# Optimization experiments

Measured on AMD Instinct MI355X. Metric: run time of the kernel, lower is better.

Reference implementation:

```python
import jax, jax.numpy as jnp
import numpy as np

EPS = 1e-5
N, K, CIN, COUT = 100000, 27, 64, 128


def sparse_conv(x, nbr, W):
    # x: [N, C]; nbr: [N, K] with sentinel index N meaning 'no neighbor'
    x_pad = jnp.concatenate([x, jnp.zeros((1, x.shape[1]), x.dtype)], axis=0)  # [N+1, C]
    g = x_pad[nbr]  # gather: [N, K, C]
    return jnp.einsum('nkc,kcd->nd', g, W)  # per-offset GEMM, scatter to output sites


def bn_relu(y, gamma, beta):
    # BatchNorm over active sites (training-mode batch statistics), then ReLU
    mu = y.mean(axis=0)
    var = y.var(axis=0)
    return jax.nn.relu((y - mu) * jax.lax.rsqrt(var + EPS) * gamma + beta)


def setup_inputs() -> dict:
    key = jax.random.key(0)
    ks = jax.random.split(key, 5)
    x = jax.random.normal(ks[0], (N, CIN), dtype=jnp.float32)
    # sentinel N indicates missing neighbor (maps to zero-padded row)
    nbr = jax.random.randint(ks[1], (N, K), 0, N + 1)
    W1 = jax.random.normal(ks[2], (K, CIN, COUT), dtype=jnp.float32) * (1.0 / np.sqrt(K * CIN))
    W2 = jax.random.normal(ks[3], (K, COUT, COUT), dtype=jnp.float32) * (1.0 / np.sqrt(K * COUT))
    W_skip = jax.random.normal(ks[4], (CIN, COUT), dtype=jnp.float32) * (1.0 / np.sqrt(CIN))
    return {
        'x': x, 'nbr': nbr,
        'W1': W1, 'gamma1': jnp.ones((COUT,), jnp.float32), 'beta1': jnp.zeros((COUT,), jnp.float32),
        'W2': W2, 'gamma2': jnp.ones((COUT,), jnp.float32), 'beta2': jnp.zeros((COUT,), jnp.float32),
        'W_skip': W_skip,
    }


def reference(x, nbr, W1, gamma1, beta1, W2, gamma2, beta2, W_skip):
    identity = x @ W_skip                      # 1x1 conv skip (same coords)
    h = bn_relu(sparse_conv(x, nbr, W1), gamma1, beta1)
    h = bn_relu(sparse_conv(h, nbr, W2), gamma2, beta2)
    return h + identity
```

## Files before the change

### kernel.cpp

```cpp
#include <hip/hip_runtime.h>
#include <hip/hip_bf16.h>

#define NSITES 100000
#define KOFFS 27
#define CIN 64
#define COUT 128

typedef unsigned short u16;
typedef __attribute__((ext_vector_type(8))) short s16x8;
typedef __attribute__((ext_vector_type(4))) float f32x4;

static __device__ __forceinline__ u16 f2bf(float f) {
    union { float f; unsigned u; } x; x.f = f;
    return (u16)((x.u + 0x7FFFu + ((x.u >> 16) & 1u)) >> 16);
}
static __device__ __forceinline__ float bf2f(u16 v) {
    union { unsigned u; float f; } x; x.u = ((unsigned)v) << 16;
    return x.f;
}

__global__ void prep_kernel(const float* __restrict__ W1, const float* __restrict__ W2,
                            const float* __restrict__ Wsk,
                            u16* __restrict__ W1t, u16* __restrict__ W2t,
                            u16* __restrict__ Wskt, float* __restrict__ zero_area) {
    int i = blockIdx.x * 256 + threadIdx.x;
    if (i < 27 * 64 * 128) {
        int k = i / 8192, r = i & 8191, d = r >> 6, c = r & 63;
        W1t[i] = f2bf(W1[k * 8192 + c * 128 + d]);
        return;
    }
    i -= 27 * 64 * 128;
    if (i < 27 * 128 * 128) {
        int k = i / 16384, r = i & 16383, d = r >> 7, c = r & 127;
        W2t[i] = f2bf(W2[k * 16384 + c * 128 + d]);
        return;
    }
    i -= 27 * 128 * 128;
    if (i < 8192) {
        int d = i >> 6, c = i & 63;
        Wskt[i] = f2bf(Wsk[c * 128 + d]);
        return;
    }
    i -= 8192;
    zero_area[i] = 0.0f;
}

__global__ void convert_x_kernel(const float* __restrict__ x, u16* __restrict__ xb) {
    long long e = ((long long)blockIdx.x * 256 + threadIdx.x) * 8;
    if (e >= (long long)(NSITES + 1) * CIN) return;
    s16x8 o;
    if (e < (long long)NSITES * CIN) {
        float4 v0 = *(const float4*)(x + e);
        float4 v1 = *(const float4*)(x + e + 4);
        o[0] = (short)f2bf(v0.x); o[1] = (short)f2bf(v0.y);
        o[2] = (short)f2bf(v0.z); o[3] = (short)f2bf(v0.w);
        o[4] = (short)f2bf(v1.x); o[5] = (short)f2bf(v1.y);
        o[6] = (short)f2bf(v1.z); o[7] = (short)f2bf(v1.w);
    } else {
#pragma unroll
        for (int j = 0; j < 8; ++j) o[j] = 0;
    }
    *(s16x8*)(xb + e) = o;
}

template <int CK, bool IDENT_FUSE, bool STATS>
__global__ __launch_bounds__(256, 3) void conv_kernel(
    const u16* __restrict__ xin, const int* __restrict__ nbr,
    const u16* __restrict__ Wt, u16* __restrict__ yout,
    float* __restrict__ psum, float* __restrict__ psq, int nk,
    const u16* __restrict__ Wskt, float* __restrict__ outid) {
    constexpr int STRIDE = CK + 8;
    constexpr int KSTEPS = CK / 32;
    constexpr int CPR = CK / 8;
    constexpr int RPP = 256 / CPR;
    constexpr int NPASS = 64 / RPP;
    __shared__ __align__(16) u16 a_tile[64 * STRIDE];
    __shared__ int nbr_tile[64 * KOFFS];

    const int tid = threadIdx.x;
    const int wave = tid >> 6;
    const int lane = tid & 63;
    const int m = lane & 15;
    const int q = lane >> 4;
    const int n0 = blockIdx.x * 64;
    const int wc = wave * 32;
    const int srow = tid / CPR;
    const int schunk = tid % CPR;

    for (int i = tid; i < 64 * KOFFS; i += 256) {
        int r = i / KOFFS;
        int kk = i - r * KOFFS;
        int row = n0 + r;
        nbr_tile[i] = (row < NSITES) ? nbr[row * KOFFS + kk] : NSITES;
    }
    __syncthreads();

    f32x4 acc[4][2];
#pragma unroll
    for (int rt = 0; rt < 4; ++rt)
#pragma unroll
        for (int ct = 0; ct < 2; ++ct)
#pragma unroll
            for (int r = 0; r < 4; ++r) acc[rt][ct][r] = 0.0f;

    s16x8 ag0[NPASS], ag1[NPASS];
#pragma unroll
    for (int p = 0; p < NPASS; ++p) {
        int r = p * RPP + srow;
        ag0[p] = *(const s16x8*)(xin + (long long)nbr_tile[r * KOFFS] * CK + schunk * 8);
    }
    if (nk > 1) {
#pragma unroll
        for (int p = 0; p < NPASS; ++p) {
            int r = p * RPP + srow;
            ag1[p] = *(const s16x8*)(xin + (long long)nbr_tile[r * KOFFS + 1] * CK + schunk * 8);
        }
    }

    auto conv_iter = [&](int k, s16x8 (&agc)[NPASS]) {
        s16x8 bf[2][KSTEPS];
        const u16* wb = Wt + (long long)k * (COUT * CK);
#pragma unroll
        for (int ct = 0; ct < 2; ++ct)
#pragma unroll
            for (int ks = 0; ks < KSTEPS; ++ks)
                bf[ct][ks] = *(const s16x8*)(wb + (wc + ct * 16 + m) * CK + ks * 32 + q * 8);

#pragma unroll
        for (int p = 0; p < NPASS; ++p)
            *(s16x8*)(a_tile + (p * RPP + srow) * STRIDE + schunk * 8) = agc[p];

        if (k + 2 < nk) {
#pragma unroll
            for (int p = 0; p < NPASS; ++p) {
                int r = p * RPP + srow;
                agc[p] = *(const s16x8*)(xin + (long long)nbr_tile[r * KOFFS + k + 2] * CK + schunk * 8);
            }
        }
        __syncthreads();

#pragma unroll
        for (int ks = 0; ks < KSTEPS; ++ks) {
            s16x8 af[4];
#pragma unroll
            for (int rt = 0; rt < 4; ++rt)
                af[rt] = *(const s16x8*)(a_tile + (rt * 16 + m) * STRIDE + ks * 32 + q * 8);
#pragma unroll
            for (int rt = 0; rt < 4; ++rt)
#pragma unroll
                for (int ct = 0; ct < 2; ++ct)
                    acc[rt][ct] = __builtin_amdgcn_mfma_f32_16x16x32_bf16(
                        af[rt], bf[ct][ks], acc[rt][ct], 0, 0, 0);
        }
        __syncthreads();
    };

    for (int k = 0; k < nk; k += 2) {
        conv_iter(k, ag0);
        if (k + 1 < nk) conv_iter(k + 1, ag1);
    }

#pragma unroll
    for (int rt = 0; rt < 4; ++rt) {
        int rowb = n0 + rt * 16 + q * 4;
#pragma unroll
        for (int ct = 0; ct < 2; ++ct) {
            int col = wc + ct * 16 + m;
#pragma unroll
            for (int r = 0; r < 4; ++r) {
                int row = rowb + r;
                if (row < NSITES) yout[(long long)row * COUT + col] = f2bf(acc[rt][ct][r]);
            }
        }
    }

    if (STATS) {
#pragma unroll
        for (int ct = 0; ct < 2; ++ct) {
            float s = 0.f, ss = 0.f;
#pragma unroll
            for (int rt = 0; rt < 4; ++rt)
#pragma unroll
                for (int r = 0; r < 4; ++r) {
                    float v = acc[rt][ct][r];
                    s += v; ss += v * v;
                }
            s += __shfl_xor(s, 16); ss += __shfl_xor(ss, 16);
            s += __shfl_xor(s, 32); ss += __shfl_xor(ss, 32);
            if (q == 0) {
                int col = wc + ct * 16 + m;
                int slot = blockIdx.x & 63;
                atomicAdd(psum + slot * COUT + col, s);
                atomicAdd(psq + slot * COUT + col, ss);
            }
        }
    }

    if (IDENT_FUSE) {
#pragma unroll
        for (int rt = 0; rt < 4; ++rt)
#pragma unroll
            for (int ct = 0; ct < 2; ++ct)
#pragma unroll
                for (int r = 0; r < 4; ++r) acc[rt][ct][r] = 0.0f;
        s16x8 aid[NPASS];
#pragma unroll
        for (int p = 0; p < NPASS; ++p) {
            int row = n0 + p * RPP + srow;
            long long idx = (row < NSITES) ? row : NSITES;
            aid[p] = *(const s16x8*)(xin + idx * CK + schunk * 8);
        }
        s16x8 bfi[2][KSTEPS];
#pragma unroll
        for (int ct = 0; ct < 2; ++ct)
#pragma unroll
            for (int ks = 0; ks < KSTEPS; ++ks)
                bfi[ct][ks] = *(const s16x8*)(Wskt + (wc + ct * 16 + m) * CK + ks * 32 + q * 8);
#pragma unroll
        for (int p = 0; p < NPASS; ++p)
            *(s16x8*)(a_tile + (p * RPP + srow) * STRIDE + schunk * 8) = aid[p];
        __syncthreads();
#pragma unroll
        for (int ks = 0; ks < KSTEPS; ++ks) {
            s16x8 af[4];
#pragma unroll
            for (int rt = 0; rt < 4; ++rt)
                af[rt] = *(const s16x8*)(a_tile + (rt * 16 + m) * STRIDE + ks * 32 + q * 8);
#pragma unroll
            for (int rt = 0; rt < 4; ++rt)
#pragma unroll
                for (int ct = 0; ct < 2; ++ct)
                    acc[rt][ct] = __builtin_amdgcn_mfma_f32_16x16x32_bf16(
                        af[rt], bfi[ct][ks], acc[rt][ct], 0, 0, 0);
        }
#pragma unroll
        for (int rt = 0; rt < 4; ++rt) {
            int rowb = n0 + rt * 16 + q * 4;
#pragma unroll
            for (int ct = 0; ct < 2; ++ct) {
                int col = wc + ct * 16 + m;
#pragma unroll
                for (int r = 0; r < 4; ++r) {
                    int row = rowb + r;
                    if (row < NSITES) outid[(long long)row * COUT + col] = acc[rt][ct][r];
                }
            }
        }
    }
}

__global__ void bn_stats_kernel(const float* __restrict__ psum, const float* __restrict__ psq,
                                const float* __restrict__ gamma, const float* __restrict__ beta,
                                float* __restrict__ ab) {
    int col = threadIdx.x;
    float s = 0.f, ss = 0.f;
    for (int i = 0; i < 64; ++i) { s += psum[i * COUT + col]; ss += psq[i * COUT + col]; }
    const float inv_n = 1.0f / (float)NSITES;
    float mu = s * inv_n;
    float var = ss * inv_n - mu * mu;
    float rs = rsqrtf(var + 1e-5f);
    float a = gamma[col] * rs;
    ab[col] = a;
    ab[COUT + col] = beta[col] - mu * a;
}

__global__ void bn_apply_kernel(const u16* __restrict__ y, const float* __restrict__ ab,
                                u16* __restrict__ h) {
    long long e = ((long long)blockIdx.x * 256 + threadIdx.x) * 8;
    if (e >= (long long)(NSITES + 1) * COUT) return;
    s16x8 o;
    if (e < (long long)NSITES * COUT) {
        int cb = (int)(e & (COUT - 1));
        s16x8 v = *(const s16x8*)(y + e);
#pragma unroll
        for (int j = 0; j < 8; ++j) {
            float r = bf2f((u16)v[j]) * ab[cb + j] + ab[COUT + cb + j];
            o[j] = (short)f2bf(fmaxf(r, 0.f));
        }
    } else {
#pragma unroll
        for (int j = 0; j < 8; ++j) o[j] = 0;
    }
    *(s16x8*)(h + e) = o;
}

__global__ void final_kernel(const u16* __restrict__ y, const float* __restrict__ ab,
                             float* __restrict__ out) {
    long long e = ((long long)blockIdx.x * 256 + threadIdx.x) * 8;
    if (e >= (long long)NSITES * COUT) return;
    int cb = (int)(e & (COUT - 1));
    s16x8 v = *(const s16x8*)(y + e);
    float4 i0 = *(const float4*)(out + e);
    float4 i1 = *(const float4*)(out + e + 4);
    float is[8] = {i0.x, i0.y, i0.z, i0.w, i1.x, i1.y, i1.z, i1.w};
    float os[8];
#pragma unroll
    for (int j = 0; j < 8; ++j) {
        float r = bf2f((u16)v[j]) * ab[cb + j] + ab[COUT + cb + j];
        os[j] = fmaxf(r, 0.f) + is[j];
    }
    *(float4*)(out + e) = make_float4(os[0], os[1], os[2], os[3]);
    *(float4*)(out + e + 4) = make_float4(os[4], os[5], os[6], os[7]);
}

extern "C" void kernel_launch(void* const* d_in, const int* in_sizes, int n_in,
                              void* d_out, int out_size, void* d_ws, size_t ws_size,
                              hipStream_t stream) {
    const float* x   = (const float*)d_in[0];
    const int*   nbr = (const int*)d_in[1];
    const float* W1  = (const float*)d_in[2];
    const float* g1  = (const float*)d_in[3];
    const float* b1  = (const float*)d_in[4];
    const float* W2  = (const float*)d_in[5];
    const float* g2  = (const float*)d_in[6];
    const float* b2  = (const float*)d_in[7];
    const float* Wsk = (const float*)d_in[8];
    float* out = (float*)d_out;

    char* ws = (char*)d_ws;
    u16*   xb   = (u16*)(ws);
    u16*   W1t  = (u16*)(ws + 12800128);
    u16*   W2t  = (u16*)(ws + 13242496);
    u16*   Wskt = (u16*)(ws + 14127232);
    u16*   y    = (u16*)(ws + 14143616);
    u16*   h1   = (u16*)(ws + 39743616);
    float* ps1  = (float*)(ws + 65343872);
    float* pq1  = ps1 + 8192;
    float* ps2  = pq1 + 8192;
    float* pq2  = ps2 + 8192;
    float* ab1  = pq2 + 8192;
    float* ab2  = ab1 + 256;

    const int NBLK = (NSITES + 63) / 64;

    prep_kernel<<<2752, 256, 0, stream>>>(W1, W2, Wsk, W1t, W2t, Wskt, ps1);
    convert_x_kernel<<<3126, 256, 0, stream>>>(x, xb);
    conv_kernel<64, true, true><<<NBLK, 256, 0, stream>>>(xb, nbr, W1t, y, ps1, pq1, KOFFS, Wskt, out);
    bn_stats_kernel<<<1, 128, 0, stream>>>(ps1, pq1, g1, b1, ab1);
    bn_apply_kernel<<<6251, 256, 0, stream>>>(y, ab1, h1);
    conv_kernel<128, false, true><<<NBLK, 256, 0, stream>>>(h1, nbr, W2t, y, ps2, pq2, KOFFS, nullptr, nullptr);
    bn_stats_kernel<<<1, 128, 0, stream>>>(ps2, pq2, g2, b2, ab2);
    final_kernel<<<6250, 256, 0, stream>>>(y, ab2, out);
}
```

Baseline: 454.6 us.

## Double-buffer the LDS A tile with one barrier per offset, raise occupancy

The gathered neighbor tile now alternates between two LDS buffers. The next offset's rows are written into the idle buffer while MFMAs read the current one, so each kernel offset needs one barrier instead of two. The barrier becomes a custom lgkmcnt wait plus s_barrier, and the register prefetch is shifted one step further ahead. The kernel also raises the launch-bounds minimum to 4 blocks and shrinks the row padding to CK+4. That padding leaves 16-byte LDS vector accesses misaligned, which may split them or cause bank conflicts, and the tighter register budget may cause spills.

```diff
diff --git a/kernel.cpp b/kernel.cpp
--- a/kernel.cpp
+++ b/kernel.cpp
@@ -17,6 +17,12 @@
 static __device__ __forceinline__ float bf2f(u16 v) {
     union { unsigned u; float f; } x; x.u = ((unsigned)v) << 16;
     return x.f;
+}
+
+static __device__ __forceinline__ void lds_barrier() {
+    asm volatile("s_waitcnt lgkmcnt(0)" ::: "memory");
+    __builtin_amdgcn_s_barrier();
+    __builtin_amdgcn_sched_barrier(0);
 }
 
 __global__ void prep_kernel(const float* __restrict__ W1, const float* __restrict__ W2,
@@ -64,17 +70,17 @@
 }
 
 template <int CK, bool IDENT_FUSE, bool STATS>
-__global__ __launch_bounds__(256, 3) void conv_kernel(
+__global__ __launch_bounds__(256, 4) void conv_kernel(
     const u16* __restrict__ xin, const int* __restrict__ nbr,
     const u16* __restrict__ Wt, u16* __restrict__ yout,
     float* __restrict__ psum, float* __restrict__ psq, int nk,
     const u16* __restrict__ Wskt, float* __restrict__ outid) {
-    constexpr int STRIDE = CK + 8;
+    constexpr int STRIDE = CK + 4;
     constexpr int KSTEPS = CK / 32;
     constexpr int CPR = CK / 8;
     constexpr int RPP = 256 / CPR;
     constexpr int NPASS = 64 / RPP;
-    __shared__ __align__(16) u16 a_tile[64 * STRIDE];
+    __shared__ __align__(16) u16 a_tile[2][64 * STRIDE];
     __shared__ int nbr_tile[64 * KOFFS];
 
     const int tid = threadIdx.x;
@@ -116,8 +122,19 @@
             ag1[p] = *(const s16x8*)(xin + (long long)nbr_tile[r * KOFFS + 1] * CK + schunk * 8);
         }
     }
-
-    auto conv_iter = [&](int k, s16x8 (&agc)[NPASS]) {
+#pragma unroll
+    for (int p = 0; p < NPASS; ++p)
+        *(s16x8*)(&a_tile[0][(p * RPP + srow) * STRIDE + schunk * 8]) = ag0[p];
+    if (nk > 2) {
+#pragma unroll
+        for (int p = 0; p < NPASS; ++p) {
+            int r = p * RPP + srow;
+            ag0[p] = *(const s16x8*)(xin + (long long)nbr_tile[r * KOFFS + 2] * CK + schunk * 8);
+        }
+    }
+    lds_barrier();
+
+    auto conv_iter = [&](int k, s16x8 (&wset)[NPASS]) {
         s16x8 bf[2][KSTEPS];
         const u16* wb = Wt + (long long)k * (COUT * CK);
 #pragma unroll
@@ -126,25 +143,26 @@
             for (int ks = 0; ks < KSTEPS; ++ks)
                 bf[ct][ks] = *(const s16x8*)(wb + (wc + ct * 16 + m) * CK + ks * 32 + q * 8);
 
-#pragma unroll
-        for (int p = 0; p < NPASS; ++p)
-            *(s16x8*)(a_tile + (p * RPP + srow) * STRIDE + schunk * 8) = agc[p];
-
-        if (k + 2 < nk) {
-#pragma unroll
-            for (int p = 0; p < NPASS; ++p) {
-                int r = p * RPP + srow;
-                agc[p] = *(const s16x8*)(xin + (long long)nbr_tile[r * KOFFS + k + 2] * CK + schunk * 8);
+        const int cur = k & 1;
+        if (k + 1 < nk) {
+#pragma unroll
+            for (int p = 0; p < NPASS; ++p)
+                *(s16x8*)(&a_tile[cur ^ 1][(p * RPP + srow) * STRIDE + schunk * 8]) = wset[p];
+            if (k + 3 < nk) {
+#pragma unroll
+                for (int p = 0; p < NPASS; ++p) {
+                    int r = p * RPP + srow;
+                    wset[p] = *(const s16x8*)(xin + (long long)nbr_tile[r * KOFFS + k + 3] * CK + schunk * 8);
+                }
             }
         }
-        __syncthreads();
 
 #pragma unroll
         for (int ks = 0; ks < KSTEPS; ++ks) {
             s16x8 af[4];
 #pragma unroll
             for (int rt = 0; rt < 4; ++rt)
-                af[rt] = *(const s16x8*)(a_tile + (rt * 16 + m) * STRIDE + ks * 32 + q * 8);
+                af[rt] = *(const s16x8*)(&a_tile[cur][(rt * 16 + m) * STRIDE + ks * 32 + q * 8]);
 #pragma unroll
             for (int rt = 0; rt < 4; ++rt)
 #pragma unroll
@@ -152,13 +170,15 @@
                     acc[rt][ct] = __builtin_amdgcn_mfma_f32_16x16x32_bf16(
                         af[rt], bf[ct][ks], acc[rt][ct], 0, 0, 0);
         }
-        __syncthreads();
+        lds_barrier();
     };
 
-    for (int k = 0; k < nk; k += 2) {
-        conv_iter(k, ag0);
-        if (k + 1 < nk) conv_iter(k + 1, ag1);
-    }
+    int k = 0;
+    for (; k + 1 < nk; k += 2) {
+        conv_iter(k, ag1);
+        conv_iter(k + 1, ag0);
+    }
+    if (k < nk) conv_iter(k, ag1);
 
 #pragma unroll
     for (int rt = 0; rt < 4; ++rt) {
@@ -218,14 +238,14 @@
                 bfi[ct][ks] = *(const s16x8*)(Wskt + (wc + ct * 16 + m) * CK + ks * 32 + q * 8);
 #pragma unroll
         for (int p = 0; p < NPASS; ++p)
-            *(s16x8*)(a_tile + (p * RPP + srow) * STRIDE + schunk * 8) = aid[p];
-        __syncthreads();
+            *(s16x8*)(&a_tile[0][(p * RPP + srow) * STRIDE + schunk * 8]) = aid[p];
+        lds_barrier();
 #pragma unroll
         for (int ks = 0; ks < KSTEPS; ++ks) {
             s16x8 af[4];
 #pragma unroll
             for (int rt = 0; rt < 4; ++rt)
-                af[rt] = *(const s16x8*)(a_tile + (rt * 16 + m) * STRIDE + ks * 32 + q * 8);
+                af[rt] = *(const s16x8*)(&a_tile[0][(rt * 16 + m) * STRIDE + ks * 32 + q * 8]);
 #pragma unroll
             for (int rt = 0; rt < 4; ++rt)
 #pragma unroll
```

Result: no change. 460.1 us (+1.2%).

## Double-buffer LDS A-tile and prefetch weights one offset ahead in sparse conv

Applied to the files above, without the earlier changes.

Restructures the per-offset loop of the gather-GEMM conv kernel. The A tile now lives in two LDS buffers, gathered rows are fetched three offsets ahead, and weight fragments are prefetched into alternating register sets. The loop is hard-unrolled for 27 offsets, uses a custom waitcnt+barrier helper, and raises wave priority around the MFMA blocks, all to hide gather and weight-load latency behind matrix math. It also shrinks the LDS row padding from 8 to 4 elements, which breaks 16-byte alignment of the 128-bit LDS row accesses. It also raises LDS use and register pressure.

```diff
diff --git a/kernel.cpp b/kernel.cpp
--- a/kernel.cpp
+++ b/kernel.cpp
@@ -17,6 +17,12 @@
 static __device__ __forceinline__ float bf2f(u16 v) {
     union { unsigned u; float f; } x; x.u = ((unsigned)v) << 16;
     return x.f;
+}
+
+static __device__ __forceinline__ void lds_barrier() {
+    asm volatile("s_waitcnt lgkmcnt(0)" ::: "memory");
+    __builtin_amdgcn_s_barrier();
+    __builtin_amdgcn_sched_barrier(0);
 }
 
 __global__ void prep_kernel(const float* __restrict__ W1, const float* __restrict__ W2,
@@ -67,14 +73,14 @@
 __global__ __launch_bounds__(256, 3) void conv_kernel(
     const u16* __restrict__ xin, const int* __restrict__ nbr,
     const u16* __restrict__ Wt, u16* __restrict__ yout,
-    float* __restrict__ psum, float* __restrict__ psq, int nk,
+    float* __restrict__ psum, float* __restrict__ psq, int nk_unused,
     const u16* __restrict__ Wskt, float* __restrict__ outid) {
-    constexpr int STRIDE = CK + 8;
+    constexpr int STRIDE = CK + 4;
     constexpr int KSTEPS = CK / 32;
     constexpr int CPR = CK / 8;
     constexpr int RPP = 256 / CPR;
     constexpr int NPASS = 64 / RPP;
-    __shared__ __align__(16) u16 a_tile[64 * STRIDE];
+    __shared__ __align__(16) u16 a_tile[2][64 * STRIDE];
     __shared__ int nbr_tile[64 * KOFFS];
 
     const int tid = threadIdx.x;
@@ -103,62 +109,78 @@
 #pragma unroll
             for (int r = 0; r < 4; ++r) acc[rt][ct][r] = 0.0f;
 
-    s16x8 ag0[NPASS], ag1[NPASS];
-#pragma unroll
-    for (int p = 0; p < NPASS; ++p) {
-        int r = p * RPP + srow;
-        ag0[p] = *(const s16x8*)(xin + (long long)nbr_tile[r * KOFFS] * CK + schunk * 8);
-    }
-    if (nk > 1) {
+    s16x8 gA[NPASS], gB[NPASS];
+    s16x8 bA[2][KSTEPS], bB[2][KSTEPS];
+
+    auto gload = [&](s16x8 (&g)[NPASS], int kk) {
 #pragma unroll
         for (int p = 0; p < NPASS; ++p) {
             int r = p * RPP + srow;
-            ag1[p] = *(const s16x8*)(xin + (long long)nbr_tile[r * KOFFS + 1] * CK + schunk * 8);
-        }
-    }
-
-    auto conv_iter = [&](int k, s16x8 (&agc)[NPASS]) {
-        s16x8 bf[2][KSTEPS];
-        const u16* wb = Wt + (long long)k * (COUT * CK);
+            g[p] = *(const s16x8*)(xin + (long long)nbr_tile[r * KOFFS + kk] * CK + schunk * 8);
+        }
+    };
+    auto bload = [&](s16x8 (&b)[2][KSTEPS], int kk) {
+        const u16* wb = Wt + (long long)kk * (COUT * CK);
 #pragma unroll
         for (int ct = 0; ct < 2; ++ct)
 #pragma unroll
             for (int ks = 0; ks < KSTEPS; ++ks)
-                bf[ct][ks] = *(const s16x8*)(wb + (wc + ct * 16 + m) * CK + ks * 32 + q * 8);
-
+                b[ct][ks] = *(const s16x8*)(wb + (wc + ct * 16 + m) * CK + ks * 32 + q * 8);
+    };
+    auto awrite = [&](s16x8 (&g)[NPASS], int buf) {
 #pragma unroll
         for (int p = 0; p < NPASS; ++p)
-            *(s16x8*)(a_tile + (p * RPP + srow) * STRIDE + schunk * 8) = agc[p];
-
-        if (k + 2 < nk) {
-#pragma unroll
-            for (int p = 0; p < NPASS; ++p) {
-                int r = p * RPP + srow;
-                agc[p] = *(const s16x8*)(xin + (long long)nbr_tile[r * KOFFS + k + 2] * CK + schunk * 8);
-            }
-        }
-        __syncthreads();
-
+            *(s16x8*)(&a_tile[buf][(p * RPP + srow) * STRIDE + schunk * 8]) = g[p];
+    };
+    auto mfma_from = [&](int buf, s16x8 (&b)[2][KSTEPS]) {
+        __builtin_amdgcn_s_setprio(1);
 #pragma unroll
         for (int ks = 0; ks < KSTEPS; ++ks) {
             s16x8 af[4];
 #pragma unroll
             for (int rt = 0; rt < 4; ++rt)
-                af[rt] = *(const s16x8*)(a_tile + (rt * 16 + m) * STRIDE + ks * 32 + q * 8);
+                af[rt] = *(const s16x8*)(&a_tile[buf][(rt * 16 + m) * STRIDE + ks * 32 + q * 8]);
 #pragma unroll
             for (int rt = 0; rt < 4; ++rt)
 #pragma unroll
                 for (int ct = 0; ct < 2; ++ct)
                     acc[rt][ct] = __builtin_amdgcn_mfma_f32_16x16x32_bf16(
-                        af[rt], bf[ct][ks], acc[rt][ct], 0, 0, 0);
-        }
-        __syncthreads();
-    };
-
-    for (int k = 0; k < nk; k += 2) {
-        conv_iter(k, ag0);
-        if (k + 1 < nk) conv_iter(k + 1, ag1);
-    }
+                        af[rt], b[ct][ks], acc[rt][ct], 0, 0, 0);
+        }
+        __builtin_amdgcn_s_setprio(0);
+    };
+
+    gload(gA, 0);
+    bload(bA, 0);
+    awrite(gA, 0);
+    gload(gA, 1);
+    bload(bB, 1);
+    gload(gB, 2);
+    lds_barrier();
+
+    auto conv_iter = [&](int k, s16x8 (&g)[NPASS], s16x8 (&bcur)[2][KSTEPS]) {
+        awrite(g, (k + 1) & 1);
+        gload(g, k + 3);
+        lds_barrier();
+        mfma_from(k & 1, bcur);
+        bload(bcur, k + 2);
+        lds_barrier();
+    };
+
+    for (int k = 0; k < 24; k += 2) {
+        conv_iter(k, gA, bA);
+        conv_iter(k + 1, gB, bB);
+    }
+    awrite(gA, 1);
+    lds_barrier();
+    mfma_from(0, bA);
+    bload(bA, 26);
+    lds_barrier();
+    awrite(gB, 0);
+    lds_barrier();
+    mfma_from(1, bB);
+    lds_barrier();
+    mfma_from(0, bA);
 
 #pragma unroll
     for (int rt = 0; rt < 4; ++rt) {
@@ -197,6 +219,7 @@
     }
 
     if (IDENT_FUSE) {
+        lds_barrier();
 #pragma unroll
         for (int rt = 0; rt < 4; ++rt)
 #pragma unroll
@@ -216,23 +239,9 @@
 #pragma unroll
             for (int ks = 0; ks < KSTEPS; ++ks)
                 bfi[ct][ks] = *(const s16x8*)(Wskt + (wc + ct * 16 + m) * CK + ks * 32 + q * 8);
-#pragma unroll
-        for (int p = 0; p < NPASS; ++p)
-            *(s16x8*)(a_tile + (p * RPP + srow) * STRIDE + schunk * 8) = aid[p];
-        __syncthreads();
-#pragma unroll
-        for (int ks = 0; ks < KSTEPS; ++ks) {
-            s16x8 af[4];
-#pragma unroll
-            for (int rt = 0; rt < 4; ++rt)
-                af[rt] = *(const s16x8*)(a_tile + (rt * 16 + m) * STRIDE + ks * 32 + q * 8);
-#pragma unroll
-            for (int rt = 0; rt < 4; ++rt)
-#pragma unroll
-                for (int ct = 0; ct < 2; ++ct)
-                    acc[rt][ct] = __builtin_amdgcn_mfma_f32_16x16x32_bf16(
-                        af[rt], bfi[ct][ks], acc[rt][ct], 0, 0, 0);
-        }
+        awrite(aid, 0);
+        lds_barrier();
+        mfma_from(0, bfi);
 #pragma unroll
         for (int rt = 0; rt < 4; ++rt) {
             int rowb = n0 + rt * 16 + q * 4;
```

Measured after the change: 446.3 us. Within noise of the previous version (-1.8%).
